# Kernel optimization log

Measured on AMD Instinct MI355X. Metric: run time of the kernel, lower is better.

The kernel has to match this reference:

```python
import jax, jax.numpy as jnp
import numpy as np

N = 1024      # params.input_dim (f1 is a square [N, N] similarity matrix)
TOPK = 16     # params.topk
B = 64        # hardcoded batch in the original reshape
W = 2 * N // B  # spatial width after reshape


def setup_inputs() -> dict:
    key = jax.random.key(0)
    k1, k2, k3 = jax.random.split(key, 3)
    f1 = jax.random.normal(k1, (N, N), dtype=jnp.float32)
    # Conv2d(in=N, out=N, kernel=(TOPK, 1)) weights, kaiming-ish scale
    conv_w = jax.random.normal(k2, (N, N, TOPK, 1), dtype=jnp.float32) * 0.01
    conv_b = jax.random.normal(k3, (N,), dtype=jnp.float32) * 0.01
    return {"f1": f1, "conv_w": conv_w, "conv_b": conv_b}


def reference(f1, conv_w, conv_b):
    # i = topk indices along last dim (largest, sorted) -> [N, TOPK]
    _, idx = jax.lax.top_k(f1, TOPK)
    # pos = f1[i]: gather rows of f1 by the topk column indices -> [N, TOPK, N]
    pos = f1[idx]
    # repeat_interleave(TOPK, dim=0).reshape(N, TOPK, -1) == each row tiled TOPK times
    rep = jnp.broadcast_to(f1[:, None, :], (N, TOPK, N))
    # cat on dim=2 -> [N, TOPK, 2N]; reshape to NCHW [B, N, TOPK, W]
    out = jnp.concatenate([rep, pos], axis=2).reshape(B, N, TOPK, W)
    # Conv2d kernel (TOPK, 1), VALID padding collapses H -> 1: [B, N, 1, W]
    y = jax.lax.conv_general_dilated(
        out, conv_w, window_strides=(1, 1), padding='VALID',
        dimension_numbers=('NCHW', 'OIHW', 'NCHW'))
    y = y + conv_b[None, :, None, None]
    return jax.nn.relu(y).reshape(N, -1)  # [N, B*W] = [N, 2N]
```

## Files before the change

kernel.cpp:

```cpp
#include <hip/hip_runtime.h>
#include <stdint.h>


#define NDIM 1024
#define TK   16
#define KPOS 8192
#define KREP 512
#define NCOL 2048

typedef unsigned short u16;
typedef uint32_t u32;
typedef u16   u16x8  __attribute__((ext_vector_type(8)));
typedef __bf16 bf16x8 __attribute__((ext_vector_type(8)));
typedef float  f32x4  __attribute__((ext_vector_type(4)));

__device__ __forceinline__ u16 f2bf(float x) {
    union { float f; unsigned u; } v; v.f = x;
    unsigned r = 0x7FFFu + ((v.u >> 16) & 1u);
    return (u16)((v.u + r) >> 16);
}

__device__ __forceinline__ void load_lds_16B(const u16* g, u16* l) {
    __builtin_amdgcn_global_load_lds(
        (__attribute__((address_space(1))) void*)(uintptr_t)g,
        (__attribute__((address_space(3))) void*)(unsigned)(uintptr_t)l,
        16, 0, 0);
}

#define PREP_TOPK 256
#define PREP_ZERO 2048
#define PREP_CONV 4096
#define PREP_W1   1024
#define PREP_F1T  256

__global__ __launch_bounds__(256) void prep_kernel(const float* __restrict__ f1,
                                                   const float* __restrict__ W,
                                                   int* __restrict__ idx,
                                                   u16* __restrict__ Wb,
                                                   u16* __restrict__ W1b,
                                                   u16* __restrict__ f1t,
                                                   float* __restrict__ out) {
    const int bid = blockIdx.x;
    const int t = threadIdx.x;
    if (bid < PREP_TOPK) {
        const int lane = t & 63;
        const int row  = bid * 4 + (t >> 6);
        float v[16];
        const float* src = f1 + row * NDIM + lane;
        #pragma unroll
        for (int j = 0; j < 16; ++j) v[j] = src[j * 64];
        for (int sel = 0; sel < TK; ++sel) {
            float best = -3.402823466e38f; int bg = 0x7fffffff;
            #pragma unroll
            for (int j = 0; j < 16; ++j)
                if (v[j] > best) { best = v[j]; bg = j * 64 + lane; }
            #pragma unroll
            for (int s = 1; s < 64; s <<= 1) {
                float ov = __shfl_xor(best, s);
                int   og = __shfl_xor(bg, s);
                if (ov > best || (ov == best && og < bg)) { best = ov; bg = og; }
            }
            if (lane == sel) idx[row * TK + sel] = bg;
            #pragma unroll
            for (int j = 0; j < 16; ++j)
                if (bg == j * 64 + lane) v[j] = -3.402823466e38f;
        }
    } else if (bid < PREP_TOPK + PREP_ZERO) {
        const int zb = bid - PREP_TOPK;
        f32x4 z = {0.f, 0.f, 0.f, 0.f};
        *(f32x4*)(out + (size_t)(zb * 256 + t) * 4) = z;
    } else if (bid < PREP_TOPK + PREP_ZERO + PREP_CONV) {
        const int tid = (bid - PREP_TOPK - PREP_ZERO) * 256 + t;
        const int o  = tid >> 10;
        const int r  = tid & 1023;
        const int kp0 = r * 8;
        const int ip  = r >> 1;
        const int kh0 = (r & 1) * 8;
        const int i = (ip >> 5) * 64 + ((ip >> 1) & 15) * 4 + (ip & 1) + 2;
        const float* src = W + (size_t)o * 16384 + i * 16 + kh0;
        float4 a = *(const float4*)(src);
        float4 b = *(const float4*)(src + 4);
        u16x8 ov;
        ov[0] = f2bf(a.x); ov[1] = f2bf(a.y); ov[2] = f2bf(a.z); ov[3] = f2bf(a.w);
        ov[4] = f2bf(b.x); ov[5] = f2bf(b.y); ov[6] = f2bf(b.z); ov[7] = f2bf(b.w);
        *(u16x8*)(Wb + (size_t)o * KPOS + kp0) = ov;
    } else if (bid < PREP_TOPK + PREP_ZERO + PREP_CONV + PREP_W1) {
        const int o = bid - PREP_TOPK - PREP_ZERO - PREP_CONV;
        const float* wrow = W + (size_t)o * 16384;
        #pragma unroll
        for (int h = 0; h < 2; ++h) {
            const int kr = h * 256 + t;
            const int nl = kr >> 5, q = (kr >> 4) & 1, kh = kr & 15;
            const float* base = wrow + (nl * 64 + q) * 16 + kh;
            float s = 0.f;
            #pragma unroll
            for (int tt = 0; tt < 16; ++tt) s += base[tt * 64];
            W1b[o * KREP + kr] = f2bf(s);
        }
    } else {
        const int gb = bid - PREP_TOPK - PREP_ZERO - PREP_CONV - PREP_W1;
        const int unit = t >> 5;
        const int w = t & 31;
        const int rq = gb * 8 + unit;
        const int row = rq >> 1, q = rq & 1;
        const float* src = f1 + row * NDIM + q * 512;
        const int swp = ((w >> 2) & 1) * 8;
        u16 tmp[16];
        #pragma unroll
        for (int kh = 0; kh < 16; ++kh)
            tmp[kh ^ swp] = f2bf(src[kh * 32 + w]);
        u16* dst = f1t + ((size_t)row * 2 + q) * 512 + w * 16;
        *(u16x8*)(dst)     = *(u16x8*)(tmp);
        *(u16x8*)(dst + 8) = *(u16x8*)(tmp + 8);
    }
}

#define BM 128
#define BN 128
#define BK 64

__global__ __launch_bounds__(256, 2) void gemm_kernel(const u16* __restrict__ Ap,
                                                      const u16* __restrict__ A1,
                                                      const u16* __restrict__ f1t,
                                                      const int* __restrict__ idx,
                                                      float* __restrict__ out) {
    __shared__ __align__(16) u16 As[BM * BK];
    __shared__ __align__(16) u16 Bs[16 * 512];
    const int f = blockIdx.x;
    int m, n, kb, kiters, astride;
    const u16* Ab;
    bool isPos;
    if (f < 512) {
        m = f >> 6; const int u = f & 63; n = u & 15;
        astride = KPOS; kb = (u >> 4) * 2048; kiters = 32; Ab = Ap; isPos = true;
    } else {
        const int g = f - 512; m = g >> 4; n = g & 15;
        astride = KREP; kb = 0; kiters = 8; Ab = A1; isPos = false;
    }
    const int t    = threadIdx.x;
    const int lane = t & 63;
    const int wave = t >> 6;
    const int wm   = (wave >> 1) * 64;
    const int wn   = (wave & 1) * 64;
    const int quad = lane >> 4;
    const int l16  = lane & 15;
    const int sw   = l16 & 7;
    const int o0 = m * BM;
    const int n0 = n * BN;
    const int nb0 = n * 4;

    f32x4 acc[4][4] = {};

    const int rA = t >> 3;
    const int c8 = t & 7;
    const int csw = (c8 ^ (rA & 7)) * 8;
    const u16* gA = Ab + (size_t)(o0 + rA) * astride + kb + csw;
    u16* lA = As + t * 8;

    for (int it = 0; it < kiters; ++it) {
        const int k0 = it * BK;
        #pragma unroll
        for (int c = 0; c < 4; ++c)
            load_lds_16B(gA + (size_t)(c * 32) * astride + k0, lA + c * 2048);

        const int ip = ((kb + k0) >> 4) + wave;
        int rows[4], qp;
        if (isPos) {
            const int nl = ip >> 5, tt = (ip >> 1) & 15;
            qp = ip & 1;
            #pragma unroll
            for (int bl = 0; bl < 4; ++bl)
                rows[bl] = idx[((nb0 + bl) * 16 + nl) * TK + tt];
        } else {
            qp = ip & 1;
            const int r0 = ip >> 1;
            #pragma unroll
            for (int bl = 0; bl < 4; ++bl)
                rows[bl] = (nb0 + bl) * 16 + r0;
        }
        #pragma unroll
        for (int bl = 0; bl < 4; ++bl)
            load_lds_16B(f1t + ((size_t)rows[bl] * 2 + qp) * 512 + lane * 8,
                         Bs + (wave * 4 + bl) * 512);
        __syncthreads();

        #pragma unroll
        for (int ks = 0; ks < 2; ++ks) {
            bf16x8 af[4], bfr[4];
            #pragma unroll
            for (int mt = 0; mt < 4; ++mt) {
                u16x8 bits = *(const u16x8*)(As + (wm + mt * 16 + l16) * BK
                                                + (((ks * 4 + quad) ^ sw) * 8));
                af[mt] = __builtin_bit_cast(bf16x8, bits);
            }
            const int ci2 = ks * 2 + (quad >> 1);
            const int qh  = quad & 1;
            #pragma unroll
            for (int nt = 0; nt < 4; ++nt) {
                const int nn = wn + nt * 16 + l16;
                const int blocf = nn >> 5, w = nn & 31;
                u16x8 bits = *(const u16x8*)(Bs + (ci2 * 4 + blocf) * 512 + w * 16
                                                + ((qh ^ ((w >> 2) & 1)) * 8));
                bfr[nt] = __builtin_bit_cast(bf16x8, bits);
            }
            #pragma unroll
            for (int mt = 0; mt < 4; ++mt)
                #pragma unroll
                for (int nt = 0; nt < 4; ++nt)
                    acc[mt][nt] = __builtin_amdgcn_mfma_f32_16x16x32_bf16(
                        af[mt], bfr[nt], acc[mt][nt], 0, 0, 0);
        }
        __syncthreads();
    }

    #pragma unroll
    for (int nt = 0; nt < 4; ++nt) {
        const int nn = n0 + wn + nt * 16 + l16;
        const int bb = nn >> 5, w = nn & 31;
        #pragma unroll
        for (int mt = 0; mt < 4; ++mt) {
            #pragma unroll
            for (int r = 0; r < 4; ++r) {
                const int o = o0 + wm + mt * 16 + quad * 4 + r;
                unsafeAtomicAdd(out + (size_t)(bb * 16 + (o >> 6)) * 2048
                                    + (o & 63) * 32 + w,
                                acc[mt][nt][r]);
            }
        }
    }
}

__global__ __launch_bounds__(256) void finalize_kernel(float* __restrict__ out,
                                                       const float* __restrict__ bias) {
    const int tid = blockIdx.x * 256 + threadIdx.x;
    const int f = tid * 4;
    const int o = ((f >> 11) & 15) * 64 + ((f & 2047) >> 5);
    const float bv = bias[o];
    float4 x = *(float4*)(out + f);
    x.x = fmaxf(x.x + bv, 0.f);
    x.y = fmaxf(x.y + bv, 0.f);
    x.z = fmaxf(x.z + bv, 0.f);
    x.w = fmaxf(x.w + bv, 0.f);
    *(float4*)(out + f) = x;
}

extern "C" void kernel_launch(void* const* d_in, const int* in_sizes, int n_in,
                              void* d_out, int out_size, void* d_ws, size_t ws_size,
                              hipStream_t stream) {
    const float* f1   = (const float*)d_in[0];
    const float* Wc   = (const float*)d_in[1];
    const float* bias = (const float*)d_in[2];
    float* out = (float*)d_out;

    int* idx = (int*)d_ws;
    u16* Wb  = (u16*)((char*)d_ws + 65536);
    u16* W1b = (u16*)((char*)d_ws + 16842752);
    u16* f1t = (u16*)((char*)d_ws + 17891328);

    prep_kernel<<<PREP_TOPK + PREP_ZERO + PREP_CONV + PREP_W1 + PREP_F1T,
                  256, 0, stream>>>(f1, Wc, idx, Wb, W1b, f1t, out);
    gemm_kernel<<<512 + 128, 256, 0, stream>>>(Wb, W1b, f1t, idx, out);
    finalize_kernel<<<(NDIM * NCOL) / (4 * 256), 256, 0, stream>>>(out, bias);
}
```

Baseline: 173.9 us.

## Double-buffer LDS tiles and cache top-k indices in shared memory

Splits the GEMM main loop into a staging lambda and double-buffers the A and B LDS tiles, so the async global-to-LDS loads for the next k-tile are issued before computing on the current one. Also preloads the block's 256 top-k gather indices into LDS once, instead of reading them from global memory every iteration. The aim is to hide global load latency behind MFMA work. The cost is doubled LDS use (about 65 KB per block), which may cut occupancy below the requested 2 blocks per CU. There is also a possible race: the next stage is written without a barrier after the previous iteration's reads, depending on where the loop-end sync sits.

After: 164.9 us. 5.2% less time.

```diff
diff --git a/kernel.cpp b/kernel.cpp
--- a/kernel.cpp
+++ b/kernel.cpp
@@ -124,8 +124,9 @@
                                                       const u16* __restrict__ f1t,
                                                       const int* __restrict__ idx,
                                                       float* __restrict__ out) {
-    __shared__ __align__(16) u16 As[BM * BK];
-    __shared__ __align__(16) u16 Bs[16 * 512];
+    __shared__ __align__(16) u16 As[2][BM * BK];
+    __shared__ __align__(16) u16 Bs[2][16 * 512];
+    __shared__ int idxL[256];
     const int f = blockIdx.x;
     int m, n, kb, kiters, astride;
     const u16* Ab;
@@ -148,6 +149,12 @@
     const int o0 = m * BM;
     const int n0 = n * BN;
     const int nb0 = n * 4;
+    const int nl0 = kb >> 9;
+
+    if (isPos) {
+        const int bl = t >> 6, nlz = (t >> 4) & 3, tt = t & 15;
+        idxL[t] = idx[((nb0 + bl) * 16 + nl0 + nlz) * TK + tt];
+    }
 
     f32x4 acc[4][4] = {};
 
@@ -155,24 +162,23 @@
     const int c8 = t & 7;
     const int csw = (c8 ^ (rA & 7)) * 8;
     const u16* gA = Ab + (size_t)(o0 + rA) * astride + kb + csw;
-    u16* lA = As + t * 8;
-
-    for (int it = 0; it < kiters; ++it) {
+    const int ipb = kb >> 4;
+
+    auto stage = [&](int it, int nb) {
         const int k0 = it * BK;
+        u16* lA = As[nb] + t * 8;
         #pragma unroll
         for (int c = 0; c < 4; ++c)
             load_lds_16B(gA + (size_t)(c * 32) * astride + k0, lA + c * 2048);
-
-        const int ip = ((kb + k0) >> 4) + wave;
-        int rows[4], qp;
+        const int ip = ipb + it * 4 + wave;
+        const int qp = ip & 1;
+        int rows[4];
         if (isPos) {
-            const int nl = ip >> 5, tt = (ip >> 1) & 15;
-            qp = ip & 1;
+            const int nlz = (ip >> 5) & 3, tt = (ip >> 1) & 15;
             #pragma unroll
             for (int bl = 0; bl < 4; ++bl)
-                rows[bl] = idx[((nb0 + bl) * 16 + nl) * TK + tt];
+                rows[bl] = idxL[bl * 64 + nlz * 16 + tt];
         } else {
-            qp = ip & 1;
             const int r0 = ip >> 1;
             #pragma unroll
             for (int bl = 0; bl < 4; ++bl)
@@ -181,15 +187,24 @@
         #pragma unroll
         for (int bl = 0; bl < 4; ++bl)
             load_lds_16B(f1t + ((size_t)rows[bl] * 2 + qp) * 512 + lane * 8,
-                         Bs + (wave * 4 + bl) * 512);
-        __syncthreads();
+                         Bs[nb] + (wave * 4 + bl) * 512);
+    };
+
+    __syncthreads();
+    stage(0, 0);
+    __syncthreads();
+
+    #pragma unroll 2
+    for (int it = 0; it < kiters; ++it) {
+        const int cur = it & 1;
+        if (it + 1 < kiters) stage(it + 1, 1 - cur);
 
         #pragma unroll
         for (int ks = 0; ks < 2; ++ks) {
             bf16x8 af[4], bfr[4];
             #pragma unroll
             for (int mt = 0; mt < 4; ++mt) {
-                u16x8 bits = *(const u16x8*)(As + (wm + mt * 16 + l16) * BK
+                u16x8 bits = *(const u16x8*)(As[cur] + (wm + mt * 16 + l16) * BK
                                                 + (((ks * 4 + quad) ^ sw) * 8));
                 af[mt] = __builtin_bit_cast(bf16x8, bits);
             }
@@ -199,7 +214,7 @@
             for (int nt = 0; nt < 4; ++nt) {
                 const int nn = wn + nt * 16 + l16;
                 const int blocf = nn >> 5, w = nn & 31;
-                u16x8 bits = *(const u16x8*)(Bs + (ci2 * 4 + blocf) * 512 + w * 16
+                u16x8 bits = *(const u16x8*)(Bs[cur] + (ci2 * 4 + blocf) * 512 + w * 16
                                                 + ((qh ^ ((w >> 2) & 1)) * 8));
                 bfr[nt] = __builtin_bit_cast(bf16x8, bits);
             }
```
